# Performance work log

Measured on AMD Instinct MI355X. Metric: run time of the kernel, lower is better.

The kernel has to match this reference:

```python
import jax, jax.numpy as jnp
import numpy as np

B, T, N, D, K = 8, 64, 512, 64, 8
d = D // K  # per-head dim
NEG = -(2.0 ** 15) + 1.0  # -32767, as in source


def setup_inputs() -> dict:
    key = jax.random.key(0)
    ks = jax.random.split(key, 12)
    s = 0.05
    inp = {
        "x": jax.random.normal(ks[0], (B, T, N, D), dtype=jnp.float32),
        "ste": jax.random.normal(ks[1], (B, T, N, D), dtype=jnp.float32),
        "Wq": jax.random.normal(ks[2], (2 * D, D), dtype=jnp.float32) * s,
        "bq": jnp.zeros((D,), dtype=jnp.float32),
        "Wk": jax.random.normal(ks[3], (2 * D, D), dtype=jnp.float32) * s,
        "bk": jnp.zeros((D,), dtype=jnp.float32),
        "Wv": jax.random.normal(ks[4], (2 * D, D), dtype=jnp.float32) * s,
        "bv": jnp.zeros((D,), dtype=jnp.float32),
        "W1": jax.random.normal(ks[5], (D, D), dtype=jnp.float32) * s,
        "b1": jnp.zeros((D,), dtype=jnp.float32),
        "W2": jax.random.normal(ks[6], (D, D), dtype=jnp.float32) * s,
        "b2": jnp.zeros((D,), dtype=jnp.float32),
    }
    return inp


def reference(x, ste, Wq, bq, Wk, bk, Wv, bv, W1, b1, W2, b2):
    h = jnp.concatenate([x, ste], axis=-1)  # (B,T,N,2D)
    q = jax.nn.relu(jnp.einsum("btnf,fd->btnd", h, Wq) + bq)
    k = jax.nn.relu(jnp.einsum("btnf,fd->btnd", h, Wk) + bk)
    v = jax.nn.relu(jnp.einsum("btnf,fd->btnd", h, Wv) + bv)
    # split D into K heads of size d (torch split/cat over batch == head axis)
    q = q.reshape(B, T, N, K, d)
    k = k.reshape(B, T, N, K, d)
    v = v.reshape(B, T, N, K, d)
    scores = jnp.einsum("btnkd,bsnkd->bnkts", q, k) / jnp.sqrt(jnp.float32(d))
    causal = jnp.tril(jnp.ones((T, T), dtype=bool))  # (T,T)
    scores = jnp.where(causal, scores, jnp.float32(NEG))
    attn = jax.nn.softmax(scores, axis=-1)  # (B,N,K,T,T)
    out = jnp.einsum("bnkts,bsnkd->btnkd", attn, v).reshape(B, T, N, D)
    out = jax.nn.relu(jnp.einsum("btnd,de->btne", out, W1) + b1)
    out = jnp.einsum("btnd,de->btne", out, W2) + b2
    return out
```

## Files before the change

kernel.cpp:

```cpp
#include <hip/hip_runtime.h>


#define Bb 8
#define Tt 64
#define Nn 512
#define Dd 64

typedef unsigned short u16;
typedef unsigned int u32;
typedef __bf16 bf16x8 __attribute__((ext_vector_type(8)));
typedef float f32x4 __attribute__((ext_vector_type(4)));
typedef short s16x8 __attribute__((ext_vector_type(8)));

#define QS 72
#define PS 72

#define WSQ 0
#define WSK 8192
#define WSV 16384
#define WS1 24576
#define WS2 28672

__device__ inline u16 f2bf(float f) {
    u32 x = __float_as_uint(f);
    x += 0x7fffu + ((x >> 16) & 1u);
    return (u16)(x >> 16);
}
__device__ inline bf16x8 ldf(const u16* p) { return *(const bf16x8*)p; }
__device__ inline bf16x8 zf8() {
    s16x8 z = {0, 0, 0, 0, 0, 0, 0, 0};
    return __builtin_bit_cast(bf16x8, z);
}
__device__ inline bf16x8 pack8(float4 a, float4 b) {
    s16x8 r;
    r[0] = (short)f2bf(a.x); r[1] = (short)f2bf(a.y);
    r[2] = (short)f2bf(a.z); r[3] = (short)f2bf(a.w);
    r[4] = (short)f2bf(b.x); r[5] = (short)f2bf(b.y);
    r[6] = (short)f2bf(b.z); r[7] = (short)f2bf(b.w);
    return __builtin_bit_cast(bf16x8, r);
}

template<int KD, int MODE, bool AREG>
__device__ inline void gemm(const bf16x8* afr,
                            const u16* aLds, int As,
                            const u16* __restrict__ WtG,
                            const float* __restrict__ bias,
                            u16* O, int Os, float* G,
                            int w, int lane, float scale) {
    const int l15 = lane & 15, qd = lane >> 4;
    f32x4 acc[4] = {{0,0,0,0},{0,0,0,0},{0,0,0,0},{0,0,0,0}};
#pragma unroll
    for (int c = 0; c < KD / 32; ++c) {
        bf16x8 af = AREG ? afr[c]
                         : ldf(&aLds[(16 * w + l15) * As + c * 32 + qd * 8]);
#pragma unroll
        for (int ct = 0; ct < 4; ++ct) {
            bf16x8 bfr = *(const bf16x8*)&WtG[(16 * ct + l15) * KD + c * 32 + qd * 8];
            acc[ct] = __builtin_amdgcn_mfma_f32_16x16x32_bf16(af, bfr, acc[ct], 0, 0, 0);
        }
    }
#pragma unroll
    for (int ct = 0; ct < 4; ++ct) {
        const int col = 16 * ct + l15;
        const float bv = bias[col];
#pragma unroll
        for (int r = 0; r < 4; ++r) {
            const int row = 16 * w + 4 * qd + r;
            float v = acc[ct][r] + bv;
            if (MODE != 2) v = fmaxf(v, 0.f);
            v *= scale;
            if (MODE == 0)      O[row * Os + col] = f2bf(v);
            else if (MODE == 1) O[col * Os + row] = f2bf(v);
            else                G[(size_t)row * (Nn * Dd) + col] = v;
        }
    }
}

__global__ __launch_bounds__(256)
void prep_w(const float* __restrict__ Wq, const float* __restrict__ Wk,
            const float* __restrict__ Wv, const float* __restrict__ W1,
            const float* __restrict__ W2, u16* __restrict__ ws) {
    int i = blockIdx.x * 256 + threadIdx.x;
    if (i < 24576) {
        int m = i >> 13;
        int r = i & 8191;
        int k = r >> 6, c = r & 63;
        const float* W = (m == 0) ? Wq : (m == 1) ? Wk : Wv;
        ws[m * 8192 + c * 128 + k] = f2bf(W[r]);
    } else if (i < 32768) {
        int j = i - 24576;
        int m = j >> 12;
        int r = j & 4095;
        int k = r >> 6, c = r & 63;
        const float* W = (m == 0) ? W1 : W2;
        ws[24576 + m * 4096 + c * 64 + k] = f2bf(W[r]);
    }
}

__global__ __launch_bounds__(256, 4)
void ta_fused_kernel(const float* __restrict__ x,  const float* __restrict__ ste,
                     const float* __restrict__ bq, const float* __restrict__ bk,
                     const float* __restrict__ bv, const float* __restrict__ b1,
                     const float* __restrict__ b2, const u16* __restrict__ ws,
                     float* __restrict__ out) {
    __shared__ __align__(16) u16 sm[18432];
    u16* qb = sm;
    u16* kb = sm + 4608;
    u16* vT = sm + 9216;
    u16* pB = sm + 13824;

    const int tid  = threadIdx.x;
    const int w    = tid >> 6;
    const int lane = tid & 63;
    const int l15  = lane & 15, qd = lane >> 4;
    const int bid  = blockIdx.x;
    const int b = bid >> 9, n = bid & 511;

    const int t = 16 * w + l15;
    const float* xr = x   + (((size_t)b * Tt + t) * Nn + n) * Dd;
    const float* sr = ste + (((size_t)b * Tt + t) * Nn + n) * Dd;
    bf16x8 af[4];
#pragma unroll
    for (int c = 0; c < 2; ++c) {
        float4 p0 = *(const float4*)(xr + c * 32 + qd * 8);
        float4 p1 = *(const float4*)(xr + c * 32 + qd * 8 + 4);
        af[c] = pack8(p0, p1);
    }
#pragma unroll
    for (int c = 0; c < 2; ++c) {
        float4 p0 = *(const float4*)(sr + c * 32 + qd * 8);
        float4 p1 = *(const float4*)(sr + c * 32 + qd * 8 + 4);
        af[c + 2] = pack8(p0, p1);
    }

    gemm<128, 0, true>(af, nullptr, 0, ws + WSQ, bq, qb, QS, nullptr, w, lane,
                       0.35355339059327373f);
    gemm<128, 0, true>(af, nullptr, 0, ws + WSK, bk, kb, QS, nullptr, w, lane, 1.f);
    gemm<128, 1, true>(af, nullptr, 0, ws + WSV, bv, vT, QS, nullptr, w, lane, 1.f);
    __syncthreads();

    u16* pb = pB + 1152 * w;
    u16* attnout = qb;
    const bf16x8 z8 = zf8();
#pragma unroll 1
    for (int h8 = 0; h8 < 64; h8 += 8) {
        bf16x8 qa = (qd == 0) ? ldf(&qb[(16 * w + l15) * QS + h8]) : z8;
        f32x4 sv[4] = {{0,0,0,0},{0,0,0,0},{0,0,0,0},{0,0,0,0}};
#pragma unroll
        for (int ct = 0; ct < 4; ++ct) {
            bf16x8 bfr = (qd == 0) ? ldf(&kb[(16 * ct + l15) * QS + h8]) : z8;
            sv[ct] = __builtin_amdgcn_mfma_f32_16x16x32_bf16(qa, bfr, sv[ct], 0, 0, 0);
        }
        const int tr = 16 * w + 4 * qd;
#pragma unroll
        for (int ct = 0; ct < 4; ++ct) {
            const int sc = 16 * ct + l15;
#pragma unroll
            for (int r = 0; r < 4; ++r)
                sv[ct][r] = (sc <= tr + r) ? __expf(sv[ct][r]) : 0.f;
        }
        f32x4 dsum = sv[0] + sv[1] + sv[2] + sv[3];
#pragma unroll
        for (int m = 1; m <= 8; m <<= 1) {
#pragma unroll
            for (int r = 0; r < 4; ++r)
                dsum[r] += __shfl_xor(dsum[r], m, 64);
        }
#pragma unroll
        for (int ct = 0; ct < 4; ++ct)
#pragma unroll
            for (int r = 0; r < 4; ++r)
                pb[(4 * qd + r) * PS + 16 * ct + l15] = f2bf(sv[ct][r]);
        f32x4 o = {0, 0, 0, 0};
#pragma unroll
        for (int k0 = 0; k0 < 64; k0 += 32) {
            bf16x8 pa = ldf(&pb[l15 * PS + k0 + qd * 8]);
            int vrow = h8 + (l15 & 7);
            bf16x8 vfr = (l15 < 8) ? ldf(&vT[vrow * QS + k0 + qd * 8]) : z8;
            o = __builtin_amdgcn_mfma_f32_16x16x32_bf16(pa, vfr, o, 0, 0, 0);
        }
        if (l15 < 8) {
#pragma unroll
            for (int r = 0; r < 4; ++r) {
                float inv = __builtin_amdgcn_rcpf(dsum[r]);
                attnout[(16 * w + 4 * qd + r) * QS + h8 + l15] = f2bf(o[r] * inv);
            }
        }
    }

    gemm<64, 0, false>(nullptr, attnout, QS, ws + WS1, b1, pB, QS, nullptr,
                       w, lane, 1.f);
    float* ob = out + (((size_t)b * Tt) * Nn + n) * Dd;
    gemm<64, 2, false>(nullptr, pB, QS, ws + WS2, b2, nullptr, 0, ob,
                       w, lane, 1.f);
}

extern "C" void kernel_launch(void* const* d_in, const int* in_sizes, int n_in,
                              void* d_out, int out_size, void* d_ws, size_t ws_size,
                              hipStream_t stream) {
    const float* x   = (const float*)d_in[0];
    const float* ste = (const float*)d_in[1];
    const float* Wq  = (const float*)d_in[2];
    const float* bq  = (const float*)d_in[3];
    const float* Wk  = (const float*)d_in[4];
    const float* bk  = (const float*)d_in[5];
    const float* Wv  = (const float*)d_in[6];
    const float* bv  = (const float*)d_in[7];
    const float* W1  = (const float*)d_in[8];
    const float* b1  = (const float*)d_in[9];
    const float* W2  = (const float*)d_in[10];
    const float* b2  = (const float*)d_in[11];
    float* out = (float*)d_out;
    u16* ws = (u16*)d_ws;

    hipLaunchKernelGGL(prep_w, dim3(128), dim3(256), 0, stream,
                       Wq, Wk, Wv, W1, W2, ws);
    hipLaunchKernelGGL(ta_fused_kernel, dim3(Bb * Nn), dim3(256), 0, stream,
                       x, ste, bq, bk, bv, b1, b2, ws, out);
}
```

Baseline: 286.9 us.

## Transpose attention MFMAs to keep probabilities in registers and skip masked tiles

The score MFMA now computes K·Qᵀ instead of Q·Kᵀ, with K rows permuted at store time. Each lane then holds a column of probabilities laid out to feed the PV MFMA directly as packed bf16 registers, so the per-head round trip through shared memory and the 16-lane shuffle reduction go away. Causally fully-masked key tiles are skipped per wave (ctmax, w>=2). The V-transpose store is vectorised as well. The cost is more complex index permutation logic and load imbalance between waves.

```diff
diff --git a/kernel.cpp b/kernel.cpp
--- a/kernel.cpp
+++ b/kernel.cpp
@@ -11,9 +11,9 @@
 typedef __bf16 bf16x8 __attribute__((ext_vector_type(8)));
 typedef float f32x4 __attribute__((ext_vector_type(4)));
 typedef short s16x8 __attribute__((ext_vector_type(8)));
+typedef u32 u32x4 __attribute__((ext_vector_type(4)));
 
 #define QS 72
-#define PS 72
 
 #define WSQ 0
 #define WSK 8192
@@ -38,6 +38,9 @@
     r[4] = (short)f2bf(b.x); r[5] = (short)f2bf(b.y);
     r[6] = (short)f2bf(b.z); r[7] = (short)f2bf(b.w);
     return __builtin_bit_cast(bf16x8, r);
+}
+__device__ inline int kperm(int row) {
+    return (row & 0x23) | ((row & 4) << 2) | ((row & 0x18) >> 1);
 }
 
 template<int KD, int MODE, bool AREG>
@@ -63,15 +66,24 @@
     for (int ct = 0; ct < 4; ++ct) {
         const int col = 16 * ct + l15;
         const float bv = bias[col];
-#pragma unroll
-        for (int r = 0; r < 4; ++r) {
-            const int row = 16 * w + 4 * qd + r;
-            float v = acc[ct][r] + bv;
-            if (MODE != 2) v = fmaxf(v, 0.f);
-            v *= scale;
-            if (MODE == 0)      O[row * Os + col] = f2bf(v);
-            else if (MODE == 1) O[col * Os + row] = f2bf(v);
-            else                G[(size_t)row * (Nn * Dd) + col] = v;
+        if (MODE == 1) {
+            ushort4 st;
+            st.x = f2bf(fmaxf(acc[ct][0] + bv, 0.f) * scale);
+            st.y = f2bf(fmaxf(acc[ct][1] + bv, 0.f) * scale);
+            st.z = f2bf(fmaxf(acc[ct][2] + bv, 0.f) * scale);
+            st.w = f2bf(fmaxf(acc[ct][3] + bv, 0.f) * scale);
+            *(ushort4*)&O[col * Os + 16 * w + 4 * qd] = st;
+        } else {
+#pragma unroll
+            for (int r = 0; r < 4; ++r) {
+                const int row = 16 * w + 4 * qd + r;
+                float v = acc[ct][r] + bv;
+                if (MODE != 2) v = fmaxf(v, 0.f);
+                v *= scale;
+                if (MODE == 0)      O[row * Os + col] = f2bf(v);
+                else if (MODE == 3) O[kperm(row) * Os + col] = f2bf(v);
+                else                G[(size_t)row * (Nn * Dd) + col] = v;
+            }
         }
     }
 }
@@ -107,7 +119,7 @@
     u16* qb = sm;
     u16* kb = sm + 4608;
     u16* vT = sm + 9216;
-    u16* pB = sm + 13824;
+    u16* ao = sm + 13824;
 
     const int tid  = threadIdx.x;
     const int w    = tid >> 6;
@@ -116,9 +128,9 @@
     const int bid  = blockIdx.x;
     const int b = bid >> 9, n = bid & 511;
 
-    const int t = 16 * w + l15;
-    const float* xr = x   + (((size_t)b * Tt + t) * Nn + n) * Dd;
-    const float* sr = ste + (((size_t)b * Tt + t) * Nn + n) * Dd;
+    const int trow = 16 * w + l15;
+    const float* xr = x   + (((size_t)b * Tt + trow) * Nn + n) * Dd;
+    const float* sr = ste + (((size_t)b * Tt + trow) * Nn + n) * Dd;
     bf16x8 af[4];
 #pragma unroll
     for (int c = 0; c < 2; ++c) {
@@ -135,63 +147,75 @@
 
     gemm<128, 0, true>(af, nullptr, 0, ws + WSQ, bq, qb, QS, nullptr, w, lane,
                        0.35355339059327373f);
-    gemm<128, 0, true>(af, nullptr, 0, ws + WSK, bk, kb, QS, nullptr, w, lane, 1.f);
+    gemm<128, 3, true>(af, nullptr, 0, ws + WSK, bk, kb, QS, nullptr, w, lane, 1.f);
     gemm<128, 1, true>(af, nullptr, 0, ws + WSV, bv, vT, QS, nullptr, w, lane, 1.f);
     __syncthreads();
 
-    u16* pb = pB + 1152 * w;
-    u16* attnout = qb;
     const bf16x8 z8 = zf8();
+    const int ctmax = (w >= 2) ? 3 : 1;
 #pragma unroll 1
     for (int h8 = 0; h8 < 64; h8 += 8) {
-        bf16x8 qa = (qd == 0) ? ldf(&qb[(16 * w + l15) * QS + h8]) : z8;
+        bf16x8 qfr = (qd == 0) ? ldf(&qb[(16 * w + l15) * QS + h8]) : z8;
         f32x4 sv[4] = {{0,0,0,0},{0,0,0,0},{0,0,0,0},{0,0,0,0}};
 #pragma unroll
         for (int ct = 0; ct < 4; ++ct) {
-            bf16x8 bfr = (qd == 0) ? ldf(&kb[(16 * ct + l15) * QS + h8]) : z8;
-            sv[ct] = __builtin_amdgcn_mfma_f32_16x16x32_bf16(qa, bfr, sv[ct], 0, 0, 0);
-        }
-        const int tr = 16 * w + 4 * qd;
+            if (ct <= ctmax) {
+                bf16x8 kfr = (qd == 0) ? ldf(&kb[(16 * ct + l15) * QS + h8]) : z8;
+                sv[ct] = __builtin_amdgcn_mfma_f32_16x16x32_bf16(kfr, qfr, sv[ct], 0, 0, 0);
+            }
+        }
+        const int t = 16 * w + l15;
+        float dsum = 0.f;
+        u32 pk[8];
 #pragma unroll
         for (int ct = 0; ct < 4; ++ct) {
-            const int sc = 16 * ct + l15;
-#pragma unroll
-            for (int r = 0; r < 4; ++r)
-                sv[ct][r] = (sc <= tr + r) ? __expf(sv[ct][r]) : 0.f;
-        }
-        f32x4 dsum = sv[0] + sv[1] + sv[2] + sv[3];
-#pragma unroll
-        for (int m = 1; m <= 8; m <<= 1) {
-#pragma unroll
-            for (int r = 0; r < 4; ++r)
-                dsum[r] += __shfl_xor(dsum[r], m, 64);
-        }
-#pragma unroll
-        for (int ct = 0; ct < 4; ++ct)
-#pragma unroll
-            for (int r = 0; r < 4; ++r)
-                pb[(4 * qd + r) * PS + 16 * ct + l15] = f2bf(sv[ct][r]);
+            if (ct <= ctmax) {
+                const int sbase = 8 * qd + 4 * (ct & 1) + 32 * (ct >> 1);
+#pragma unroll
+                for (int r = 0; r < 4; ++r) {
+                    float e = (sbase + r <= t) ? __expf(sv[ct][r]) : 0.f;
+                    sv[ct][r] = e;
+                    dsum += e;
+                }
+                pk[2 * ct]     = (u32)f2bf(sv[ct][0]) | ((u32)f2bf(sv[ct][1]) << 16);
+                pk[2 * ct + 1] = (u32)f2bf(sv[ct][2]) | ((u32)f2bf(sv[ct][3]) << 16);
+            } else {
+                pk[2 * ct] = 0; pk[2 * ct + 1] = 0;
+            }
+        }
+        dsum += __shfl_xor(dsum, 16, 64);
+        dsum += __shfl_xor(dsum, 32, 64);
+
+        const int vrow = h8 + (l15 & 7);
         f32x4 o = {0, 0, 0, 0};
-#pragma unroll
-        for (int k0 = 0; k0 < 64; k0 += 32) {
-            bf16x8 pa = ldf(&pb[l15 * PS + k0 + qd * 8]);
-            int vrow = h8 + (l15 & 7);
-            bf16x8 vfr = (l15 < 8) ? ldf(&vT[vrow * QS + k0 + qd * 8]) : z8;
-            o = __builtin_amdgcn_mfma_f32_16x16x32_bf16(pa, vfr, o, 0, 0, 0);
-        }
-        if (l15 < 8) {
-#pragma unroll
-            for (int r = 0; r < 4; ++r) {
-                float inv = __builtin_amdgcn_rcpf(dsum[r]);
-                attnout[(16 * w + 4 * qd + r) * QS + h8 + l15] = f2bf(o[r] * inv);
-            }
-        }
-    }
-
-    gemm<64, 0, false>(nullptr, attnout, QS, ws + WS1, b1, pB, QS, nullptr,
+        {
+            bf16x8 va0 = ldf(&vT[vrow * QS + 0 + qd * 8]);
+            u32x4 pb0 = {pk[0], pk[1], pk[2], pk[3]};
+            o = __builtin_amdgcn_mfma_f32_16x16x32_bf16(
+                    va0, __builtin_bit_cast(bf16x8, pb0), o, 0, 0, 0);
+        }
+        if (w >= 2) {
+            bf16x8 va1 = ldf(&vT[vrow * QS + 32 + qd * 8]);
+            u32x4 pb1 = {pk[4], pk[5], pk[6], pk[7]};
+            o = __builtin_amdgcn_mfma_f32_16x16x32_bf16(
+                    va1, __builtin_bit_cast(bf16x8, pb1), o, 0, 0, 0);
+        }
+        float invd = __builtin_amdgcn_rcpf(dsum);
+        if (qd < 2) {
+            ushort4 st;
+            st.x = f2bf(o[0] * invd);
+            st.y = f2bf(o[1] * invd);
+            st.z = f2bf(o[2] * invd);
+            st.w = f2bf(o[3] * invd);
+            *(ushort4*)&ao[(16 * w + l15) * QS + h8 + 4 * qd] = st;
+        }
+    }
+
+    u16* abuf = qb;
+    gemm<64, 0, false>(nullptr, ao, QS, ws + WS1, b1, abuf, QS, nullptr,
                        w, lane, 1.f);
     float* ob = out + (((size_t)b * Tt) * Nn + n) * Dd;
-    gemm<64, 2, false>(nullptr, pB, QS, ws + WS2, b2, nullptr, 0, ob,
+    gemm<64, 2, false>(nullptr, abuf, QS, ws + WS2, b2, nullptr, 0, ob,
                        w, lane, 1.f);
 }
 
```

After: 288.6 us. About the same (+0.6%).
